# Kernel optimization log

Hardware: AMD Instinct MI355X
Metric: run time of the kernel (lower is better)

## Reference

```python
import jax, jax.numpy as jnp
import numpy as np

N = 50000
E = 1600000

def setup_inputs() -> dict:
    key = jax.random.key(0)
    ks = jax.random.split(key, 8)
    x = jax.random.normal(ks[0], (N, 512), dtype=jnp.float32)
    edge_index = jax.random.randint(ks[1], (2, E), 0, N, dtype=jnp.int32).astype(jnp.int64)
    eigenvectors = jax.random.normal(ks[2], (N, 128), dtype=jnp.float32)
    W1 = jax.random.normal(ks[3], (512, 128), dtype=jnp.float32) * 0.04
    b1 = jnp.zeros((128,), dtype=jnp.float32)
    W2 = jax.random.normal(ks[4], (128, 64), dtype=jnp.float32) * 0.09
    b2 = jnp.zeros((64,), dtype=jnp.float32)
    lin_W = jax.random.normal(ks[5], (128, 64), dtype=jnp.float32) * 0.09
    W3 = jax.random.normal(ks[6], (128, 40), dtype=jnp.float32) * 0.09
    b3 = jnp.zeros((40,), dtype=jnp.float32)
    return {"x": x, "edge_index": edge_index, "eigenvectors": eigenvectors,
            "W1": W1, "b1": b1, "W2": W2, "b2": b2, "lin_W": lin_W, "W3": W3, "b3": b3}

def _gcn_norm(edge_index, num_nodes):
    # add self loops, then symmetric normalization D^-1/2 (A+I) D^-1/2
    loop = jnp.arange(num_nodes, dtype=edge_index.dtype)
    row = jnp.concatenate([edge_index[0], loop])  # source
    col = jnp.concatenate([edge_index[1], loop])  # target
    w = jnp.ones(row.shape[0], dtype=jnp.float32)
    deg = jax.ops.segment_sum(w, col, num_segments=num_nodes)
    dis = jnp.where(deg > 0, 1.0 / jnp.sqrt(deg), 0.0)
    norm = dis[row] * dis[col]  # [E+N]
    return row, col, norm

def _gcn_conv(h, W, b, row, col, norm, num_nodes):
    h = h @ W                                  # [N, d_out] linear first (PyG order)
    msg = h[row] * norm[:, None]               # gather + scale, [E+N, d_out]
    out = jax.ops.segment_sum(msg, col, num_segments=num_nodes)  # scatter-add
    return out + b

def reference(x, edge_index, eigenvectors, W1, b1, W2, b2, lin_W, W3, b3):
    num_nodes = x.shape[0]
    row, col, norm = _gcn_norm(edge_index, num_nodes)
    h = jax.nn.relu(_gcn_conv(x, W1, b1, row, col, norm, num_nodes))
    # dropout omitted: eval mode (deterministic reference)
    h = jax.nn.relu(_gcn_conv(h, W2, b2, row, col, norm, num_nodes))
    xp = eigenvectors @ lin_W                  # Linear(spec_in, spec_out, bias=False)
    h = jnp.concatenate([h, xp], axis=1)       # [N, h2+spec_out]
    h = _gcn_conv(h, W3, b3, row, col, norm, num_nodes)
    return jax.nn.log_softmax(h, axis=1)
```

## Files before the change

### kernel.cpp

```cpp
#include <hip/hip_runtime.h>
#include <cstdint>
#include <cstddef>

constexpr int BLK = 256;
constexpr int NB = 128;

static inline size_t ws_align(size_t x) { return (x + 255) & ~size_t(255); }

typedef __attribute__((ext_vector_type(8))) short bf16x8;
typedef __attribute__((ext_vector_type(4))) float f32x4;

__device__ inline unsigned short f2bf(float f) {
  unsigned int u = __float_as_uint(f);
  unsigned int r = (u + 0x7fffu + ((u >> 16) & 1u)) >> 16;
  return (unsigned short)r;
}
__device__ inline float bf2f(unsigned short u) {
  return __uint_as_float(((unsigned int)u) << 16);
}
__device__ inline float bf2f_lo(unsigned int w) {
  return __uint_as_float(w << 16);
}
__device__ inline float bf2f_hi(unsigned int w) {
  return __uint_as_float(w & 0xffff0000u);
}

__device__ inline void gload16(const void* gp, void* lp) {
  __builtin_amdgcn_global_load_lds(
      (const __attribute__((address_space(1))) void*)gp,
      (__attribute__((address_space(3))) void*)lp, 16, 0, 0);
}

__global__ void k_pack_wt(const int* __restrict__ ei, unsigned int* __restrict__ pk,
                          int* __restrict__ cnt, int E, int nChunk,
                          const float* __restrict__ W1, const float* __restrict__ W2,
                          const float* __restrict__ linW, const float* __restrict__ W3,
                          unsigned short* __restrict__ WT1, unsigned short* __restrict__ WT2,
                          unsigned short* __restrict__ WTl, unsigned short* __restrict__ WT3) {
  if (blockIdx.x >= NB) {
    int i = (blockIdx.x - NB) * BLK + threadIdx.x;
    if (i < 65536) {
      int n = i >> 9, kg = i & 511;
      int tile = kg >> 5, k = kg & 31;
      WT1[tile * 4096 + n * 32 + k] = f2bf(W1[(size_t)kg * 128 + n]);
    } else if (i < 73728) {
      int j = i - 65536; int n = j >> 7, k = j & 127;
      WT2[j] = f2bf(W2[(size_t)k * 64 + n]);
    } else if (i < 81920) {
      int j = i - 73728; int n = j >> 7, k = j & 127;
      WTl[j] = f2bf(linW[(size_t)k * 64 + n]);
    } else if (i < 88064) {
      int j = i - 81920; int n = j >> 7, k = j & 127;
      WT3[j] = f2bf(n < 40 ? W3[(size_t)k * 40 + n] : 0.f);
    }
    return;
  }
  __shared__ int hist[256];
  for (int t = threadIdx.x; t < 256; t += BLK) hist[t] = 0;
  __syncthreads();
  int allz = 1;
  #pragma unroll 8
  for (int i = 0; i < 32; ++i) allz &= (ei[2 * i + 1] == 0) ? 1 : 0;
  const bool i64 = allz != 0;
  int beg = blockIdx.x * nChunk, end = min(beg + nChunk, E);
  for (int i = beg + threadIdx.x; i < end; i += BLK) {
    int row, col;
    if (i64) { row = ei[2 * i]; col = ei[2 * (E + i)]; }
    else     { row = ei[i];     col = ei[E + i]; }
    unsigned int p = ((unsigned int)col << 16) | (unsigned int)row;
    pk[i] = p;
    atomicAdd(&hist[col >> 8], 1);
  }
  __syncthreads();
  for (int t = threadIdx.x; t < 256; t += BLK) cnt[blockIdx.x * 256 + t] = hist[t];
}

__global__ void k_wscan(const int* __restrict__ cnt, int* __restrict__ woffs,
                        int* __restrict__ base, int nb, int E) {
  __shared__ int wsums[5];
  int w = threadIdx.x;
  int s = 0;
  for (int b = 0; b < nb; ++b) s += cnt[b * 256 + w];
  int lane = w & 63, wv = w >> 6;
  int x = s;
  #pragma unroll
  for (int sh = 1; sh < 64; sh <<= 1) { int t = __shfl_up(x, sh); if (lane >= sh) x += t; }
  if (lane == 63) wsums[wv] = x;
  __syncthreads();
  if (w == 0) { int a = 0; for (int k = 0; k < 4; ++k) { int t = wsums[k]; wsums[k] = a; a += t; } }
  __syncthreads();
  int excl = x - s + wsums[wv];
  woffs[w] = excl;
  if (w == 255) woffs[256] = excl + s;
  int start = excl;
  for (int b = 0; b < nb; ++b) { base[b * 256 + w] = start; start += cnt[b * 256 + w]; }
}

__global__ __launch_bounds__(256)
void k_part_gemm1(const unsigned int* __restrict__ pk, const int* __restrict__ base,
                  unsigned int* __restrict__ P, int E, int nChunk,
                  const float* __restrict__ x, const unsigned short* __restrict__ WT,
                  unsigned short* __restrict__ C, int N, int gG1) {
  __shared__ __align__(16) char smem[49152];
  if ((int)blockIdx.x >= gG1) {
    const int pb = (int)blockIdx.x - gG1;
    int* cur = (int*)smem;
    for (int t = threadIdx.x; t < 256; t += BLK) cur[t] = base[pb * 256 + t];
    __syncthreads();
    int beg = pb * nChunk, end = min(beg + nChunk, E);
    for (int i = beg + threadIdx.x; i < end; i += BLK) {
      unsigned int p = pk[i];
      int pos = atomicAdd(&cur[p >> 24], 1);
      P[pos] = p;
    }
    return;
  }
  float* As0 = (float*)smem;
  unsigned short* Wsl0 = (unsigned short*)(smem + 24576);
  const int tid = threadIdx.x;
  const int lane = tid & 63, wv = tid >> 6;
  const int m = lane & 15, kq = lane >> 4;
  const int row0 = (int)blockIdx.x * 64;

  const int r8 = lane >> 3;
  const int c8 = lane & 7;
  int agrow[2];
  #pragma unroll
  for (int jj = 0; jj < 2; ++jj) {
    int gr = row0 + wv * 16 + jj * 8 + r8;
    agrow[jj] = gr < N ? gr : N - 1;
  }

  f32x4 acc[8];
  #pragma unroll
  for (int t = 0; t < 8; ++t) acc[t] = {0.f, 0.f, 0.f, 0.f};

  auto STAGE = [&](int pb, int kb) {
    #pragma unroll
    for (int jj = 0; jj < 2; ++jj) {
      const float* src = x + (size_t)agrow[jj] * 512 + kb * 32 + (c8 ^ r8) * 4;
      gload16(src, As0 + pb * 2048 + (wv * 16 + jj * 8) * 32);
    }
    #pragma unroll
    for (int jj = 0; jj < 2; ++jj) {
      const unsigned short* src = WT + (size_t)kb * 4096 + wv * 1024 + jj * 512;
      gload16(src, Wsl0 + pb * 4096 + wv * 1024 + jj * 512);
    }
  };

  STAGE(0, 0);
  int cur = 0;
  #pragma unroll 1
  for (int t = 0; t < 16; ++t) {
    int nxt = cur + 1; if (nxt == 3) nxt = 0;
    if (t < 15) {
      STAGE(nxt, t + 1);
      asm volatile("s_waitcnt vmcnt(4)" ::: "memory");
    } else {
      asm volatile("s_waitcnt vmcnt(0)" ::: "memory");
    }
    __builtin_amdgcn_s_barrier();
    __builtin_amdgcn_sched_barrier(0);

    const char* Ab = (const char*)(As0 + cur * 2048);
    const char* Wb = (const char*)(Wsl0 + cur * 4096);
    const int row = wv * 16 + m;
    const int s = row & 7;
    f32x4 lo = *(const f32x4*)(Ab + row * 128 + ((kq * 2) ^ s) * 16);
    f32x4 hi = *(const f32x4*)(Ab + row * 128 + ((kq * 2 + 1) ^ s) * 16);
    bf16x8 af;
    af[0] = (short)f2bf(lo[0]); af[1] = (short)f2bf(lo[1]);
    af[2] = (short)f2bf(lo[2]); af[3] = (short)f2bf(lo[3]);
    af[4] = (short)f2bf(hi[0]); af[5] = (short)f2bf(hi[1]);
    af[6] = (short)f2bf(hi[2]); af[7] = (short)f2bf(hi[3]);
    #pragma unroll
    for (int tt = 0; tt < 8; ++tt) {
      int wrow = tt * 16 + m;
      bf16x8 bf = *(const bf16x8*)(Wb + wrow * 64 + kq * 16);
      acc[tt] = __builtin_amdgcn_mfma_f32_16x16x32_bf16(af, bf, acc[tt], 0, 0, 0);
    }
    cur = nxt;
  }

  #pragma unroll
  for (int r = 0; r < 4; ++r) {
    int rr = row0 + wv * 16 + kq * 4 + r;
    if (rr < N) {
      #pragma unroll
      for (int t = 0; t < 8; ++t)
        C[(size_t)rr * 128 + t * 16 + m] = f2bf(acc[t][r]);
    }
  }
}

__global__ void k_window_build(const unsigned int* __restrict__ P,
                               const int* __restrict__ woffs,
                               float* __restrict__ dis, int* __restrict__ offs,
                               int* __restrict__ csr, int N, int E) {
  __shared__ int hist[256];
  __shared__ int wsums[5];
  __shared__ int lbase[256];
  const int node0 = blockIdx.x * 256;
  const int t = threadIdx.x;
  hist[t] = 0;
  __syncthreads();
  const int beg = woffs[blockIdx.x], end = woffs[blockIdx.x + 1];
  for (int i = beg + t; i < end; i += BLK)
    atomicAdd(&hist[(P[i] >> 16) & 255], 1);
  __syncthreads();
  const int dg = hist[t];
  if (node0 + t < N) dis[node0 + t] = 1.0f / sqrtf((float)(dg + 1));
  int lane = t & 63, wv = t >> 6;
  int x = dg;
  #pragma unroll
  for (int sh = 1; sh < 64; sh <<= 1) { int q = __shfl_up(x, sh); if (lane >= sh) x += q; }
  if (lane == 63) wsums[wv] = x;
  __syncthreads();
  if (t == 0) { int a = 0; for (int k = 0; k < 4; ++k) { int q = wsums[k]; wsums[k] = a; a += q; } }
  __syncthreads();
  const int goff = beg + (x - dg + wsums[wv]);
  if (node0 + t < N) offs[node0 + t] = goff;
  lbase[t] = goff;
  __syncthreads();
  for (int i = beg + t; i < end; i += BLK) {
    unsigned int p = P[i];
    int pos = atomicAdd(&lbase[(p >> 16) & 255], 1);
    csr[pos] = (int)(p & 0xffffu);
  }
  if (blockIdx.x == 0 && t == 0) offs[N] = E;
}

template<int NT, int MR, bool AF32>
__device__ inline void mgemm_body(int bi, const void* __restrict__ Av,
                                  const unsigned short* __restrict__ WT,
                                  const float* __restrict__ dis, unsigned short* __restrict__ C,
                                  int ldc, int NOUT, int N) {
  constexpr int K = 128;
  const int tid = threadIdx.x;
  const int lane = tid & 63;
  const int wv = tid >> 6;
  const int m = lane & 15;
  const int kq = lane >> 4;
  const int orow = bi * (64 * MR) + wv * (16 * MR);

  int rowc[MR];
  #pragma unroll
  for (int mr = 0; mr < MR; ++mr) {
    int row = orow + mr * 16 + m;
    rowc[mr] = row < N ? row : N - 1;
  }

  f32x4 acc[MR][NT];
  #pragma unroll
  for (int mr = 0; mr < MR; ++mr)
    #pragma unroll
    for (int t = 0; t < NT; ++t) acc[mr][t] = {0.f, 0.f, 0.f, 0.f};

  #pragma unroll 4
  for (int k0 = 0; k0 < K; k0 += 32) {
    bf16x8 af[MR];
    #pragma unroll
    for (int mr = 0; mr < MR; ++mr) {
      if constexpr (AF32) {
        const float* Arow = (const float*)Av + (size_t)rowc[mr] * K + kq * 8 + k0;
        float4 a0 = *(const float4*)Arow;
        float4 a1 = *(const float4*)(Arow + 4);
        af[mr][0] = (short)f2bf(a0.x); af[mr][1] = (short)f2bf(a0.y);
        af[mr][2] = (short)f2bf(a0.z); af[mr][3] = (short)f2bf(a0.w);
        af[mr][4] = (short)f2bf(a1.x); af[mr][5] = (short)f2bf(a1.y);
        af[mr][6] = (short)f2bf(a1.z); af[mr][7] = (short)f2bf(a1.w);
      } else {
        const unsigned short* Arow = (const unsigned short*)Av + (size_t)rowc[mr] * K + kq * 8 + k0;
        af[mr] = *(const bf16x8*)Arow;
      }
    }
    bf16x8 bf[NT];
    #pragma unroll
    for (int t = 0; t < NT; ++t)
      bf[t] = *(const bf16x8*)(WT + (size_t)(t * 16 + m) * K + k0 + kq * 8);
    #pragma unroll
    for (int t = 0; t < NT; ++t)
      #pragma unroll
      for (int mr = 0; mr < MR; ++mr)
        acc[mr][t] = __builtin_amdgcn_mfma_f32_16x16x32_bf16(af[mr], bf[t], acc[mr][t], 0, 0, 0);
  }
  #pragma unroll
  for (int mr = 0; mr < MR; ++mr) {
    #pragma unroll
    for (int r = 0; r < 4; ++r) {
      int rr = orow + mr * 16 + kq * 4 + r;
      if (rr < N) {
        float s = dis ? dis[rr] : 1.f;
        #pragma unroll
        for (int t = 0; t < NT; ++t) {
          int cc = t * 16 + m;
          if (cc < NOUT)
            C[(size_t)rr * ldc + cc] = f2bf(acc[mr][t][r] * s);
        }
      }
    }
  }
}

__global__ __launch_bounds__(256)
void k_mgemm2x(const unsigned short* __restrict__ G, const unsigned short* __restrict__ WT2,
               const float* __restrict__ dis, unsigned short* __restrict__ F,
               const float* __restrict__ eig, const unsigned short* __restrict__ WTl,
               unsigned short* __restrict__ XP, int N, int nA) {
  if ((int)blockIdx.x < nA)
    mgemm_body<4, 2, false>(blockIdx.x, G, WT2, dis, F, 64, 64, N);
  else
    mgemm_body<4, 2, true>(blockIdx.x - nA, eig, WTl, nullptr, XP, 64, 64, N);
}

__global__ __launch_bounds__(256)
void k_mgemm3(const unsigned short* __restrict__ H2, const unsigned short* __restrict__ XP,
              const unsigned short* __restrict__ WT3, const float* __restrict__ dis,
              unsigned short* __restrict__ C, int N) {
  constexpr int NT = 3, MR = 2;
  const int tid = threadIdx.x;
  const int lane = tid & 63;
  const int wv = tid >> 6;
  const int m = lane & 15;
  const int kq = lane >> 4;
  const int orow = blockIdx.x * (64 * MR) + wv * (16 * MR);

  int rowc[MR];
  #pragma unroll
  for (int mr = 0; mr < MR; ++mr) {
    int row = orow + mr * 16 + m;
    rowc[mr] = row < N ? row : N - 1;
  }

  f32x4 acc[MR][NT];
  #pragma unroll
  for (int mr = 0; mr < MR; ++mr)
    #pragma unroll
    for (int t = 0; t < NT; ++t) acc[mr][t] = {0.f, 0.f, 0.f, 0.f};

  #pragma unroll 4
  for (int k0 = 0; k0 < 128; k0 += 32) {
    const unsigned short* Abase = (k0 < 64) ? H2 : XP;
    const int kk = (k0 & 63) + kq * 8;
    bf16x8 af[MR];
    #pragma unroll
    for (int mr = 0; mr < MR; ++mr)
      af[mr] = *(const bf16x8*)(Abase + (size_t)rowc[mr] * 64 + kk);
    bf16x8 bf[NT];
    #pragma unroll
    for (int t = 0; t < NT; ++t)
      bf[t] = *(const bf16x8*)(WT3 + (size_t)(t * 16 + m) * 128 + k0 + kq * 8);
    #pragma unroll
    for (int t = 0; t < NT; ++t)
      #pragma unroll
      for (int mr = 0; mr < MR; ++mr)
        acc[mr][t] = __builtin_amdgcn_mfma_f32_16x16x32_bf16(af[mr], bf[t], acc[mr][t], 0, 0, 0);
  }
  #pragma unroll
  for (int mr = 0; mr < MR; ++mr) {
    #pragma unroll
    for (int r = 0; r < 4; ++r) {
      int rr = orow + mr * 16 + kq * 4 + r;
      if (rr < N) {
        float s = dis[rr];
        #pragma unroll
        for (int t = 0; t < NT; ++t) {
          int cc = t * 16 + m;
          if (cc < 40)
            C[(size_t)rr * 40 + cc] = f2bf(acc[mr][t][r] * s);
        }
      }
    }
  }
}

template<int D, bool RELU, bool GDIS>
__launch_bounds__(BLK)
__global__ void k_agg2(const unsigned short* __restrict__ g, int ldg,
                       const float* __restrict__ dis, const float* __restrict__ bias,
                       const int* __restrict__ offs, const int* __restrict__ csr,
                       unsigned short* __restrict__ dst, int ldd, int N) {
  constexpr int CPL = D / 32;
  int wid = (blockIdx.x * BLK + threadIdx.x) >> 6;
  int lane = threadIdx.x & 63;
  if (wid >= N) return;
  const int l5 = lane >> 5, c = lane & 31;
  const float dv = dis[wid];
  float acc[CPL];
  #pragma unroll
  for (int k = 0; k < CPL; ++k) acc[k] = 0.f;

  auto addrow = [&](int r, float w) {
    if constexpr (CPL == 4) {
      uint2 v = *(const uint2*)&g[(size_t)r * ldg + c * 4];
      acc[0] = fmaf(w, bf2f_lo(v.x), acc[0]); acc[1] = fmaf(w, bf2f_hi(v.x), acc[1]);
      acc[2] = fmaf(w, bf2f_lo(v.y), acc[2]); acc[3] = fmaf(w, bf2f_hi(v.y), acc[3]);
    } else {
      unsigned int v = *(const unsigned int*)&g[(size_t)r * ldg + c * 2];
      acc[0] = fmaf(w, bf2f_lo(v), acc[0]); acc[1] = fmaf(w, bf2f_hi(v), acc[1]);
    }
  };

  if (l5 == 0) addrow(wid, GDIS ? dv : 1.0f);
  int beg = offs[wid], end = offs[wid + 1];
  for (int e0 = beg; e0 < end; e0 += 64) {
    int cnt = end - e0; if (cnt > 64) cnt = 64;
    int u = (lane < cnt) ? csr[e0 + lane] : 0;
    float du = 1.0f;
    if constexpr (GDIS) du = (lane < cnt) ? dis[u] : 0.f;
    int j = 0;
    for (; j + 3 < cnt; j += 4) {
      int r0 = __shfl(u, j + l5);
      int r1 = __shfl(u, j + 2 + l5);
      float w0 = GDIS ? __shfl(du, j + l5) : 1.0f;
      float w1 = GDIS ? __shfl(du, j + 2 + l5) : 1.0f;
      addrow(r0, w0); addrow(r1, w1);
    }
    for (; j < cnt; j += 2) {
      int jj = j + l5;
      int si = jj < cnt ? jj : j;
      int r0 = __shfl(u, si);
      float w0 = GDIS ? __shfl(du, si) : 1.0f;
      if (jj < cnt) addrow(r0, w0);
    }
  }
  #pragma unroll
  for (int k = 0; k < CPL; ++k) acc[k] += __shfl_xor(acc[k], 32);

  if (l5 == 0) {
    float o[CPL];
    #pragma unroll
    for (int k = 0; k < CPL; ++k) {
      o[k] = dv * acc[k] + bias[c * CPL + k];
      if constexpr (RELU) o[k] = fmaxf(o[k], 0.f);
    }
    if constexpr (CPL == 4) {
      uint2 pw;
      pw.x = (unsigned)f2bf(o[0]) | ((unsigned)f2bf(o[1]) << 16);
      pw.y = (unsigned)f2bf(o[2]) | ((unsigned)f2bf(o[3]) << 16);
      *(uint2*)&dst[(size_t)wid * ldd + c * 4] = pw;
    } else {
      unsigned int pw = (unsigned)f2bf(o[0]) | ((unsigned)f2bf(o[1]) << 16);
      *(unsigned int*)&dst[(size_t)wid * ldd + c * 2] = pw;
    }
  }
}

__launch_bounds__(BLK)
__global__ void k_agg40(const unsigned short* __restrict__ g,
                        const float* __restrict__ dis, const float* __restrict__ bias,
                        const int* __restrict__ offs, const int* __restrict__ csr,
                        float* __restrict__ dst, int N) {
  int wid = (blockIdx.x * BLK + threadIdx.x) >> 6;
  int lane = threadIdx.x & 63;
  if (wid >= N) return;
  const int l5 = lane >> 5, c = lane & 31;
  const bool act = c < 20;
  float a0 = 0.f, a1 = 0.f;
  auto addrow = [&](int r) {
    if (act) {
      unsigned int w = *(const unsigned int*)&g[(size_t)r * 40 + c * 2];
      a0 += bf2f_lo(w); a1 += bf2f_hi(w);
    }
  };
  if (l5 == 0) addrow(wid);
  int beg = offs[wid], end = offs[wid + 1];
  for (int e0 = beg; e0 < end; e0 += 64) {
    int cnt = end - e0; if (cnt > 64) cnt = 64;
    int u = (lane < cnt) ? csr[e0 + lane] : 0;
    int j = 0;
    for (; j + 3 < cnt; j += 4) {
      int r0 = __shfl(u, j + l5);
      int r1 = __shfl(u, j + 2 + l5);
      addrow(r0); addrow(r1);
    }
    for (; j < cnt; j += 2) {
      int jj = j + l5;
      int r0 = __shfl(u, jj < cnt ? jj : j);
      if (jj < cnt) addrow(r0);
    }
  }
  a0 += __shfl_xor(a0, 32);
  a1 += __shfl_xor(a1, 32);

  if (l5 == 0) {
    float dv = dis[wid];
    float o0 = act ? dv * a0 + bias[c * 2]     : -__builtin_inff();
    float o1 = act ? dv * a1 + bias[c * 2 + 1] : -__builtin_inff();
    float mx = fmaxf(o0, o1);
    #pragma unroll
    for (int s = 16; s >= 1; s >>= 1) mx = fmaxf(mx, __shfl_down(mx, s, 32));
    mx = __shfl(mx, 0, 32);
    float ex = act ? (expf(o0 - mx) + expf(o1 - mx)) : 0.f;
    #pragma unroll
    for (int s = 16; s >= 1; s >>= 1) ex += __shfl_down(ex, s, 32);
    float ls = logf(__shfl(ex, 0, 32));
    if (act) {
      float2 r = make_float2(o0 - mx - ls, o1 - mx - ls);
      *(float2*)&dst[(size_t)wid * 40 + c * 2] = r;
    }
  }
}

extern "C" void kernel_launch(void* const* d_in, const int* in_sizes, int n_in,
                              void* d_out, int out_size, void* d_ws, size_t ws_size,
                              hipStream_t stream) {
  const float* x    = (const float*)d_in[0];
  const int*   ei   = (const int*)d_in[1];
  const float* eig  = (const float*)d_in[2];
  const float* W1   = (const float*)d_in[3];
  const float* b1   = (const float*)d_in[4];
  const float* W2   = (const float*)d_in[5];
  const float* b2   = (const float*)d_in[6];
  const float* linW = (const float*)d_in[7];
  const float* W3   = (const float*)d_in[8];
  const float* b3   = (const float*)d_in[9];
  float* out = (float*)d_out;

  const int N = in_sizes[0] / 512;
  const int E = in_sizes[1] / 2;

  char* ws = (char*)d_ws;
  size_t off = 0;
  auto alloc = [&](size_t bytes) { char* p = ws + off; off = ws_align(off + bytes); return p; };
  unsigned int* pk = (unsigned int*)alloc((size_t)E * 4);
  unsigned int* P  = (unsigned int*)alloc((size_t)E * 4);
  int*   csr    = (int*)alloc((size_t)E * 4);
  int*   offs   = (int*)alloc((size_t)(N + 1) * 4);
  int*   cnt    = (int*)alloc((size_t)NB * 256 * 4);
  int*   base   = (int*)alloc((size_t)NB * 256 * 4);
  int*   woffs  = (int*)alloc(257 * 4);
  float* dis    = (float*)alloc((size_t)N * 4);
  unsigned short* F  = (unsigned short*)alloc((size_t)N * 128 * 2);
  unsigned short* G  = (unsigned short*)alloc((size_t)N * 128 * 2);
  unsigned short* XP = (unsigned short*)alloc((size_t)N * 64 * 2);
  unsigned short* H2 = (unsigned short*)alloc((size_t)N * 64 * 2);
  unsigned short* WT1 = (unsigned short*)alloc(128 * 512 * 2);
  unsigned short* WT2 = (unsigned short*)alloc(64 * 128 * 2);
  unsigned short* WTl = (unsigned short*)alloc(64 * 128 * 2);
  unsigned short* WT3 = (unsigned short*)alloc(48 * 128 * 2);

  const int nChunk = (E + NB - 1) / NB;
  const int NW = (N + 255) / 256;
  const int WTB = (88064 + BLK - 1) / BLK;
  const int gG1 = (N + 63) / 64;
  const int gA = (N + 3) / 4;

  k_pack_wt<<<NB + WTB, BLK, 0, stream>>>(ei, pk, cnt, E, nChunk,
                                          W1, W2, linW, W3, WT1, WT2, WTl, WT3);
  k_wscan<<<1, 256, 0, stream>>>(cnt, woffs, base, NB, E);
  k_part_gemm1<<<gG1 + NB, BLK, 0, stream>>>(pk, base, P, E, nChunk, x, WT1, F, N, gG1);
  k_window_build<<<NW, BLK, 0, stream>>>(P, woffs, dis, offs, csr, N, E);

  k_agg2<128, true, true><<<gA, BLK, 0, stream>>>(F, 128, dis, b1, offs, csr, G, 128, N);
  k_mgemm2x<<<2 * ((N + 127) / 128), BLK, 0, stream>>>(G, WT2, dis, F, eig, WTl, XP, N, (N + 127) / 128);
  k_agg2<64, true, false><<<gA, BLK, 0, stream>>>(F, 64, dis, b2, offs, csr, H2, 64, N);
  k_mgemm3<<<(N + 127) / 128, BLK, 0, stream>>>(H2, XP, WT3, dis, F, N);
  k_agg40<<<gA, BLK, 0, stream>>>(F, dis, b3, offs, csr, out, N);
}
```

Baseline: 286.8 us.

## Fold spectral linear into W3 and compute eigenvector projection early in gemm1 launch

Precomputes linW·W3[64:] as a combined 128x40 weight so the eigenvector branch becomes eig·(linW·W3b), removing the separate 64-wide XP projection and halving the K of the third GEMM. The eig projection blocks are appended to the gemm1/partition launch so they overlap with edge partitioning, and mgemm2 now only does the G·W2 work. The third GEMM adds the precomputed XP3 in its epilogue. The folded weight is computed with a naive fp32 dot product in the scan kernel, and the extra bf16 rounding of XP3 changes numerics slightly.

```diff
diff --git a/kernel.cpp b/kernel.cpp
--- a/kernel.cpp
+++ b/kernel.cpp
@@ -34,9 +34,9 @@
 __global__ void k_pack_wt(const int* __restrict__ ei, unsigned int* __restrict__ pk,
                           int* __restrict__ cnt, int E, int nChunk,
                           const float* __restrict__ W1, const float* __restrict__ W2,
-                          const float* __restrict__ linW, const float* __restrict__ W3,
+                          const float* __restrict__ W3,
                           unsigned short* __restrict__ WT1, unsigned short* __restrict__ WT2,
-                          unsigned short* __restrict__ WTl, unsigned short* __restrict__ WT3) {
+                          unsigned short* __restrict__ W3aT) {
   if (blockIdx.x >= NB) {
     int i = (blockIdx.x - NB) * BLK + threadIdx.x;
     if (i < 65536) {
@@ -46,12 +46,9 @@
     } else if (i < 73728) {
       int j = i - 65536; int n = j >> 7, k = j & 127;
       WT2[j] = f2bf(W2[(size_t)k * 64 + n]);
-    } else if (i < 81920) {
-      int j = i - 73728; int n = j >> 7, k = j & 127;
-      WTl[j] = f2bf(linW[(size_t)k * 64 + n]);
-    } else if (i < 88064) {
-      int j = i - 81920; int n = j >> 7, k = j & 127;
-      WT3[j] = f2bf(n < 40 ? W3[(size_t)k * 40 + n] : 0.f);
+    } else if (i < 76800) {
+      int j2 = i - 73728; int jj = j2 >> 6, k = j2 & 63;
+      W3aT[j2] = f2bf(jj < 40 ? W3[(size_t)k * 40 + jj] : 0.f);
     }
     return;
   }
@@ -75,8 +72,25 @@
   for (int t = threadIdx.x; t < 256; t += BLK) cnt[blockIdx.x * 256 + t] = hist[t];
 }
 
-__global__ void k_wscan(const int* __restrict__ cnt, int* __restrict__ woffs,
-                        int* __restrict__ base, int nb, int E) {
+__global__ void k_wscan_w3c(const int* __restrict__ cnt, int* __restrict__ woffs,
+                            int* __restrict__ base, int nb, int E,
+                            const float* __restrict__ linW, const float* __restrict__ W3,
+                            unsigned short* __restrict__ WT3c) {
+  if (blockIdx.x > 0) {
+    int jbase = ((int)blockIdx.x - 1) * 12;
+    for (int idx = threadIdx.x; idx < 12 * 128; idx += BLK) {
+      int j = jbase + (idx >> 7), k = idx & 127;
+      if (j >= 48) continue;
+      float v = 0.f;
+      if (j < 40) {
+        const float* lrow = linW + (size_t)k * 64;
+        #pragma unroll 8
+        for (int t = 0; t < 64; ++t) v += lrow[t] * W3[(size_t)(64 + t) * 40 + j];
+      }
+      WT3c[(size_t)j * 128 + k] = f2bf(v);
+    }
+    return;
+  }
   __shared__ int wsums[5];
   int w = threadIdx.x;
   int s = 0;
@@ -94,140 +108,6 @@
   if (w == 255) woffs[256] = excl + s;
   int start = excl;
   for (int b = 0; b < nb; ++b) { base[b * 256 + w] = start; start += cnt[b * 256 + w]; }
-}
-
-__global__ __launch_bounds__(256)
-void k_part_gemm1(const unsigned int* __restrict__ pk, const int* __restrict__ base,
-                  unsigned int* __restrict__ P, int E, int nChunk,
-                  const float* __restrict__ x, const unsigned short* __restrict__ WT,
-                  unsigned short* __restrict__ C, int N, int gG1) {
-  __shared__ __align__(16) char smem[49152];
-  if ((int)blockIdx.x >= gG1) {
-    const int pb = (int)blockIdx.x - gG1;
-    int* cur = (int*)smem;
-    for (int t = threadIdx.x; t < 256; t += BLK) cur[t] = base[pb * 256 + t];
-    __syncthreads();
-    int beg = pb * nChunk, end = min(beg + nChunk, E);
-    for (int i = beg + threadIdx.x; i < end; i += BLK) {
-      unsigned int p = pk[i];
-      int pos = atomicAdd(&cur[p >> 24], 1);
-      P[pos] = p;
-    }
-    return;
-  }
-  float* As0 = (float*)smem;
-  unsigned short* Wsl0 = (unsigned short*)(smem + 24576);
-  const int tid = threadIdx.x;
-  const int lane = tid & 63, wv = tid >> 6;
-  const int m = lane & 15, kq = lane >> 4;
-  const int row0 = (int)blockIdx.x * 64;
-
-  const int r8 = lane >> 3;
-  const int c8 = lane & 7;
-  int agrow[2];
-  #pragma unroll
-  for (int jj = 0; jj < 2; ++jj) {
-    int gr = row0 + wv * 16 + jj * 8 + r8;
-    agrow[jj] = gr < N ? gr : N - 1;
-  }
-
-  f32x4 acc[8];
-  #pragma unroll
-  for (int t = 0; t < 8; ++t) acc[t] = {0.f, 0.f, 0.f, 0.f};
-
-  auto STAGE = [&](int pb, int kb) {
-    #pragma unroll
-    for (int jj = 0; jj < 2; ++jj) {
-      const float* src = x + (size_t)agrow[jj] * 512 + kb * 32 + (c8 ^ r8) * 4;
-      gload16(src, As0 + pb * 2048 + (wv * 16 + jj * 8) * 32);
-    }
-    #pragma unroll
-    for (int jj = 0; jj < 2; ++jj) {
-      const unsigned short* src = WT + (size_t)kb * 4096 + wv * 1024 + jj * 512;
-      gload16(src, Wsl0 + pb * 4096 + wv * 1024 + jj * 512);
-    }
-  };
-
-  STAGE(0, 0);
-  int cur = 0;
-  #pragma unroll 1
-  for (int t = 0; t < 16; ++t) {
-    int nxt = cur + 1; if (nxt == 3) nxt = 0;
-    if (t < 15) {
-      STAGE(nxt, t + 1);
-      asm volatile("s_waitcnt vmcnt(4)" ::: "memory");
-    } else {
-      asm volatile("s_waitcnt vmcnt(0)" ::: "memory");
-    }
-    __builtin_amdgcn_s_barrier();
-    __builtin_amdgcn_sched_barrier(0);
-
-    const char* Ab = (const char*)(As0 + cur * 2048);
-    const char* Wb = (const char*)(Wsl0 + cur * 4096);
-    const int row = wv * 16 + m;
-    const int s = row & 7;
-    f32x4 lo = *(const f32x4*)(Ab + row * 128 + ((kq * 2) ^ s) * 16);
-    f32x4 hi = *(const f32x4*)(Ab + row * 128 + ((kq * 2 + 1) ^ s) * 16);
-    bf16x8 af;
-    af[0] = (short)f2bf(lo[0]); af[1] = (short)f2bf(lo[1]);
-    af[2] = (short)f2bf(lo[2]); af[3] = (short)f2bf(lo[3]);
-    af[4] = (short)f2bf(hi[0]); af[5] = (short)f2bf(hi[1]);
-    af[6] = (short)f2bf(hi[2]); af[7] = (short)f2bf(hi[3]);
-    #pragma unroll
-    for (int tt = 0; tt < 8; ++tt) {
-      int wrow = tt * 16 + m;
-      bf16x8 bf = *(const bf16x8*)(Wb + wrow * 64 + kq * 16);
-      acc[tt] = __builtin_amdgcn_mfma_f32_16x16x32_bf16(af, bf, acc[tt], 0, 0, 0);
-    }
-    cur = nxt;
-  }
-
-  #pragma unroll
-  for (int r = 0; r < 4; ++r) {
-    int rr = row0 + wv * 16 + kq * 4 + r;
-    if (rr < N) {
-      #pragma unroll
-      for (int t = 0; t < 8; ++t)
-        C[(size_t)rr * 128 + t * 16 + m] = f2bf(acc[t][r]);
-    }
-  }
-}
-
-__global__ void k_window_build(const unsigned int* __restrict__ P,
-                               const int* __restrict__ woffs,
-                               float* __restrict__ dis, int* __restrict__ offs,
-                               int* __restrict__ csr, int N, int E) {
-  __shared__ int hist[256];
-  __shared__ int wsums[5];
-  __shared__ int lbase[256];
-  const int node0 = blockIdx.x * 256;
-  const int t = threadIdx.x;
-  hist[t] = 0;
-  __syncthreads();
-  const int beg = woffs[blockIdx.x], end = woffs[blockIdx.x + 1];
-  for (int i = beg + t; i < end; i += BLK)
-    atomicAdd(&hist[(P[i] >> 16) & 255], 1);
-  __syncthreads();
-  const int dg = hist[t];
-  if (node0 + t < N) dis[node0 + t] = 1.0f / sqrtf((float)(dg + 1));
-  int lane = t & 63, wv = t >> 6;
-  int x = dg;
-  #pragma unroll
-  for (int sh = 1; sh < 64; sh <<= 1) { int q = __shfl_up(x, sh); if (lane >= sh) x += q; }
-  if (lane == 63) wsums[wv] = x;
-  __syncthreads();
-  if (t == 0) { int a = 0; for (int k = 0; k < 4; ++k) { int q = wsums[k]; wsums[k] = a; a += q; } }
-  __syncthreads();
-  const int goff = beg + (x - dg + wsums[wv]);
-  if (node0 + t < N) offs[node0 + t] = goff;
-  lbase[t] = goff;
-  __syncthreads();
-  for (int i = beg + t; i < end; i += BLK) {
-    unsigned int p = P[i];
-    int pos = atomicAdd(&lbase[(p >> 16) & 255], 1);
-    csr[pos] = (int)(p & 0xffffu);
-  }
-  if (blockIdx.x == 0 && t == 0) offs[N] = E;
 }
 
 template<int NT, int MR, bool AF32>
@@ -303,21 +183,156 @@
 }
 
 __global__ __launch_bounds__(256)
-void k_mgemm2x(const unsigned short* __restrict__ G, const unsigned short* __restrict__ WT2,
-               const float* __restrict__ dis, unsigned short* __restrict__ F,
-               const float* __restrict__ eig, const unsigned short* __restrict__ WTl,
-               unsigned short* __restrict__ XP, int N, int nA) {
-  if ((int)blockIdx.x < nA)
-    mgemm_body<4, 2, false>(blockIdx.x, G, WT2, dis, F, 64, 64, N);
-  else
-    mgemm_body<4, 2, true>(blockIdx.x - nA, eig, WTl, nullptr, XP, 64, 64, N);
+void k_part_gemm1(const unsigned int* __restrict__ pk, const int* __restrict__ base,
+                  unsigned int* __restrict__ P, int E, int nChunk,
+                  const float* __restrict__ x, const unsigned short* __restrict__ WT,
+                  unsigned short* __restrict__ C, int N, int gG1,
+                  const float* __restrict__ eig, const unsigned short* __restrict__ WT3c,
+                  unsigned short* __restrict__ XP3) {
+  __shared__ __align__(16) char smem[49152];
+  if ((int)blockIdx.x >= gG1 + NB) {
+    mgemm_body<3, 2, true>((int)blockIdx.x - gG1 - NB, eig, WT3c, nullptr, XP3, 40, 40, N);
+    return;
+  }
+  if ((int)blockIdx.x >= gG1) {
+    const int pb = (int)blockIdx.x - gG1;
+    int* cur = (int*)smem;
+    for (int t = threadIdx.x; t < 256; t += BLK) cur[t] = base[pb * 256 + t];
+    __syncthreads();
+    int beg = pb * nChunk, end = min(beg + nChunk, E);
+    for (int i = beg + threadIdx.x; i < end; i += BLK) {
+      unsigned int p = pk[i];
+      int pos = atomicAdd(&cur[p >> 24], 1);
+      P[pos] = p;
+    }
+    return;
+  }
+  float* As0 = (float*)smem;
+  unsigned short* Wsl0 = (unsigned short*)(smem + 24576);
+  const int tid = threadIdx.x;
+  const int lane = tid & 63, wv = tid >> 6;
+  const int m = lane & 15, kq = lane >> 4;
+  const int row0 = (int)blockIdx.x * 64;
+
+  const int r8 = lane >> 3;
+  const int c8 = lane & 7;
+  int agrow[2];
+  #pragma unroll
+  for (int jj = 0; jj < 2; ++jj) {
+    int gr = row0 + wv * 16 + jj * 8 + r8;
+    agrow[jj] = gr < N ? gr : N - 1;
+  }
+
+  f32x4 acc[8];
+  #pragma unroll
+  for (int t = 0; t < 8; ++t) acc[t] = {0.f, 0.f, 0.f, 0.f};
+
+  auto STAGE = [&](int pb, int kb) {
+    #pragma unroll
+    for (int jj = 0; jj < 2; ++jj) {
+      const float* src = x + (size_t)agrow[jj] * 512 + kb * 32 + (c8 ^ r8) * 4;
+      gload16(src, As0 + pb * 2048 + (wv * 16 + jj * 8) * 32);
+    }
+    #pragma unroll
+    for (int jj = 0; jj < 2; ++jj) {
+      const unsigned short* src = WT + (size_t)kb * 4096 + wv * 1024 + jj * 512;
+      gload16(src, Wsl0 + pb * 4096 + wv * 1024 + jj * 512);
+    }
+  };
+
+  STAGE(0, 0);
+  int cur = 0;
+  #pragma unroll 1
+  for (int t = 0; t < 16; ++t) {
+    int nxt = cur + 1; if (nxt == 3) nxt = 0;
+    if (t < 15) {
+      STAGE(nxt, t + 1);
+      asm volatile("s_waitcnt vmcnt(4)" ::: "memory");
+    } else {
+      asm volatile("s_waitcnt vmcnt(0)" ::: "memory");
+    }
+    __builtin_amdgcn_s_barrier();
+    __builtin_amdgcn_sched_barrier(0);
+
+    const char* Ab = (const char*)(As0 + cur * 2048);
+    const char* Wb = (const char*)(Wsl0 + cur * 4096);
+    const int row = wv * 16 + m;
+    const int s = row & 7;
+    f32x4 lo = *(const f32x4*)(Ab + row * 128 + ((kq * 2) ^ s) * 16);
+    f32x4 hi = *(const f32x4*)(Ab + row * 128 + ((kq * 2 + 1) ^ s) * 16);
+    bf16x8 af;
+    af[0] = (short)f2bf(lo[0]); af[1] = (short)f2bf(lo[1]);
+    af[2] = (short)f2bf(lo[2]); af[3] = (short)f2bf(lo[3]);
+    af[4] = (short)f2bf(hi[0]); af[5] = (short)f2bf(hi[1]);
+    af[6] = (short)f2bf(hi[2]); af[7] = (short)f2bf(hi[3]);
+    #pragma unroll
+    for (int tt = 0; tt < 8; ++tt) {
+      int wrow = tt * 16 + m;
+      bf16x8 bf = *(const bf16x8*)(Wb + wrow * 64 + kq * 16);
+      acc[tt] = __builtin_amdgcn_mfma_f32_16x16x32_bf16(af, bf, acc[tt], 0, 0, 0);
+    }
+    cur = nxt;
+  }
+
+  #pragma unroll
+  for (int r = 0; r < 4; ++r) {
+    int rr = row0 + wv * 16 + kq * 4 + r;
+    if (rr < N) {
+      #pragma unroll
+      for (int t = 0; t < 8; ++t)
+        C[(size_t)rr * 128 + t * 16 + m] = f2bf(acc[t][r]);
+    }
+  }
+}
+
+__global__ void k_window_build(const unsigned int* __restrict__ P,
+                               const int* __restrict__ woffs,
+                               float* __restrict__ dis, int* __restrict__ offs,
+                               int* __restrict__ csr, int N, int E) {
+  __shared__ int hist[256];
+  __shared__ int wsums[5];
+  __shared__ int lbase[256];
+  const int node0 = blockIdx.x * 256;
+  const int t = threadIdx.x;
+  hist[t] = 0;
+  __syncthreads();
+  const int beg = woffs[blockIdx.x], end = woffs[blockIdx.x + 1];
+  for (int i = beg + t; i < end; i += BLK)
+    atomicAdd(&hist[(P[i] >> 16) & 255], 1);
+  __syncthreads();
+  const int dg = hist[t];
+  if (node0 + t < N) dis[node0 + t] = 1.0f / sqrtf((float)(dg + 1));
+  int lane = t & 63, wv = t >> 6;
+  int x = dg;
+  #pragma unroll
+  for (int sh = 1; sh < 64; sh <<= 1) { int q = __shfl_up(x, sh); if (lane >= sh) x += q; }
+  if (lane == 63) wsums[wv] = x;
+  __syncthreads();
+  if (t == 0) { int a = 0; for (int k = 0; k < 4; ++k) { int q = wsums[k]; wsums[k] = a; a += q; } }
+  __syncthreads();
+  const int goff = beg + (x - dg + wsums[wv]);
+  if (node0 + t < N) offs[node0 + t] = goff;
+  lbase[t] = goff;
+  __syncthreads();
+  for (int i = beg + t; i < end; i += BLK) {
+    unsigned int p = P[i];
+    int pos = atomicAdd(&lbase[(p >> 16) & 255], 1);
+    csr[pos] = (int)(p & 0xffffu);
+  }
+  if (blockIdx.x == 0 && t == 0) offs[N] = E;
 }
 
 __global__ __launch_bounds__(256)
-void k_mgemm3(const unsigned short* __restrict__ H2, const unsigned short* __restrict__ XP,
-              const unsigned short* __restrict__ WT3, const float* __restrict__ dis,
-              unsigned short* __restrict__ C, int N) {
-  constexpr int NT = 3, MR = 2;
+void k_mgemm2(const unsigned short* __restrict__ G, const unsigned short* __restrict__ WT2,
+              const float* __restrict__ dis, unsigned short* __restrict__ F2, int N) {
+  mgemm_body<4, 2, false>(blockIdx.x, G, WT2, dis, F2, 64, 64, N);
+}
+
+__global__ __launch_bounds__(256)
+void k_mgemm3b(const unsigned short* __restrict__ H2, const unsigned short* __restrict__ W3aT,
+               const unsigned short* __restrict__ XP3, const float* __restrict__ dis,
+               unsigned short* __restrict__ F3, int N) {
+  constexpr int NT = 3, MR = 2, K = 64;
   const int tid = threadIdx.x;
   const int lane = tid & 63;
   const int wv = tid >> 6;
@@ -338,18 +353,16 @@
     #pragma unroll
     for (int t = 0; t < NT; ++t) acc[mr][t] = {0.f, 0.f, 0.f, 0.f};
 
-  #pragma unroll 4
-  for (int k0 = 0; k0 < 128; k0 += 32) {
-    const unsigned short* Abase = (k0 < 64) ? H2 : XP;
-    const int kk = (k0 & 63) + kq * 8;
+  #pragma unroll
+  for (int k0 = 0; k0 < K; k0 += 32) {
     bf16x8 af[MR];
     #pragma unroll
     for (int mr = 0; mr < MR; ++mr)
-      af[mr] = *(const bf16x8*)(Abase + (size_t)rowc[mr] * 64 + kk);
+      af[mr] = *(const bf16x8*)(H2 + (size_t)rowc[mr] * 64 + kq * 8 + k0);
     bf16x8 bf[NT];
     #pragma unroll
     for (int t = 0; t < NT; ++t)
-      bf[t] = *(const bf16x8*)(WT3 + (size_t)(t * 16 + m) * 128 + k0 + kq * 8);
+      bf[t] = *(const bf16x8*)(W3aT + (size_t)(t * 16 + m) * 64 + k0 + kq * 8);
     #pragma unroll
     for (int t = 0; t < NT; ++t)
       #pragma unroll
@@ -366,8 +379,10 @@
         #pragma unroll
         for (int t = 0; t < NT; ++t) {
           int cc = t * 16 + m;
-          if (cc < 40)
-            C[(size_t)rr * 40 + cc] = f2bf(acc[mr][t][r] * s);
+          if (cc < 40) {
+            float xpv = bf2f(XP3[(size_t)rr * 40 + cc]);
+            F3[(size_t)rr * 40 + cc] = f2bf((acc[mr][t][r] + xpv) * s);
+          }
         }
       }
     }
@@ -531,30 +546,34 @@
   int*   base   = (int*)alloc((size_t)NB * 256 * 4);
   int*   woffs  = (int*)alloc(257 * 4);
   float* dis    = (float*)alloc((size_t)N * 4);
-  unsigned short* F  = (unsigned short*)alloc((size_t)N * 128 * 2);
-  unsigned short* G  = (unsigned short*)alloc((size_t)N * 128 * 2);
-  unsigned short* XP = (unsigned short*)alloc((size_t)N * 64 * 2);
-  unsigned short* H2 = (unsigned short*)alloc((size_t)N * 64 * 2);
+  unsigned short* F   = (unsigned short*)alloc((size_t)N * 128 * 2);
+  unsigned short* G   = (unsigned short*)alloc((size_t)N * 128 * 2);
+  unsigned short* F2  = (unsigned short*)alloc((size_t)N * 64 * 2);
+  unsigned short* H2  = (unsigned short*)alloc((size_t)N * 64 * 2);
+  unsigned short* XP3 = (unsigned short*)alloc((size_t)N * 40 * 2);
+  unsigned short* F3  = (unsigned short*)alloc((size_t)N * 40 * 2);
   unsigned short* WT1 = (unsigned short*)alloc(128 * 512 * 2);
   unsigned short* WT2 = (unsigned short*)alloc(64 * 128 * 2);
-  unsigned short* WTl = (unsigned short*)alloc(64 * 128 * 2);
-  unsigned short* WT3 = (unsigned short*)alloc(48 * 128 * 2);
+  unsigned short* W3aT = (unsigned short*)alloc(48 * 64 * 2);
+  unsigned short* WT3c = (unsigned short*)alloc(48 * 128 * 2);
 
   const int nChunk = (E + NB - 1) / NB;
   const int NW = (N + 255) / 256;
-  const int WTB = (88064 + BLK - 1) / BLK;
+  const int WTB = (76800 + BLK - 1) / BLK;
   const int gG1 = (N + 63) / 64;
+  const int gX  = (N + 127) / 128;
   const int gA = (N + 3) / 4;
 
   k_pack_wt<<<NB + WTB, BLK, 0, stream>>>(ei, pk, cnt, E, nChunk,
-                                          W1, W2, linW, W3, WT1, WT2, WTl, WT3);
-  k_wscan<<<1, 256, 0, stream>>>(cnt, woffs, base, NB, E);
-  k_part_gemm1<<<gG1 + NB, BLK, 0, stream>>>(pk, base, P, E, nChunk, x, WT1, F, N, gG1);
+                                          W1, W2, W3, WT1, WT2, W3aT);
+  k_wscan_w3c<<<5, 256, 0, stream>>>(cnt, woffs, base, NB, E, linW, W3, WT3c);
+  k_part_gemm1<<<gG1 + NB + gX, BLK, 0, stream>>>(pk, base, P, E, nChunk, x, WT1, F, N, gG1,
+                                                  eig, WT3c, XP3);
   k_window_build<<<NW, BLK, 0, stream>>>(P, woffs, dis, offs, csr, N, E);
 
   k_agg2<128, true, true><<<gA, BLK, 0, stream>>>(F, 128, dis, b1, offs, csr, G, 128, N);
-  k_mgemm2x<<<2 * ((N + 127) / 128), BLK, 0, stream>>>(G, WT2, dis, F, eig, WTl, XP, N, (N + 127) / 128);
-  k_agg2<64, true, false><<<gA, BLK, 0, stream>>>(F, 64, dis, b2, offs, csr, H2, 64, N);
-  k_mgemm3<<<(N + 127) / 128, BLK, 0, stream>>>(H2, XP, WT3, dis, F, N);
-  k_agg40<<<gA, BLK, 0, stream>>>(F, dis, b3, offs, csr, out, N);
-}
+  k_mgemm2<<<gX, BLK, 0, stream>>>(G, WT2, dis, F2, N);
+  k_agg2<64, true, false><<<gA, BLK, 0, stream>>>(F2, 64, dis, b2, offs, csr, H2, 64, N);
+  k_mgemm3b<<<gX, BLK, 0, stream>>>(H2, W3aT, XP3, dis, F3, N);
+  k_agg40<<<gA, BLK, 0, stream>>>(F3, dis, b3, offs, csr, out, N);
+}
```

Measured after the change: 280.0 us. 2.4% less time.
